# Kernel optimization log

Measured on AMD Instinct MI355X. Metric: run time of the kernel, lower is better.

Reference implementation:

```python
import jax, jax.numpy as jnp
import numpy as np

N_NODES = 100000
N_EDGES = 3200000
EPS = 1e-5


def gcn_conv(x, edge_index, W, b):
    # PyG GCNConv: sym-normalized A+I, transform-then-propagate
    h = x @ W                                   # [N, out]
    src, dst = edge_index[0], edge_index[1]
    ones = jnp.ones(edge_index.shape[1], dtype=x.dtype)
    deg = jax.ops.segment_sum(ones, dst, num_segments=N_NODES) + 1.0  # +1 self-loop
    dis = jax.lax.rsqrt(deg)                    # deg^{-1/2}
    coef = (dis[src] * dis[dst])[:, None]
    agg = jax.ops.segment_sum(h[src] * coef, dst, num_segments=N_NODES)
    agg = agg + h * (dis * dis)[:, None]        # self-loop contribution
    return agg + b


def batch_norm(x, gamma, beta):
    mu = jnp.mean(x, axis=0)
    var = jnp.mean(jnp.square(x - mu), axis=0)
    return (x - mu) * jax.lax.rsqrt(var + EPS) * gamma + beta


def setup_inputs() -> dict:
    key = jax.random.key(0)
    ks = jax.random.split(key, 12)
    d = {
        "x": jax.random.normal(ks[0], (N_NODES, 256), dtype=jnp.float32),
        "edge_index": jax.random.randint(ks[1], (2, N_EDGES), 0, N_NODES, dtype=jnp.int32),
        "W1": jax.random.normal(ks[2], (256, 128), dtype=jnp.float32) * (1.0 / np.sqrt(256)),
        "b1": jnp.zeros((128,), jnp.float32),
        "g1": jnp.ones((128,), jnp.float32),
        "bt1": jnp.zeros((128,), jnp.float32),
        "W2": jax.random.normal(ks[3], (128, 64), dtype=jnp.float32) * (1.0 / np.sqrt(128)),
        "b2": jnp.zeros((64,), jnp.float32),
        "g2": jnp.ones((64,), jnp.float32),
        "bt2": jnp.zeros((64,), jnp.float32),
        "W3": jax.random.normal(ks[4], (64, 32), dtype=jnp.float32) * (1.0 / np.sqrt(64)),
        "b3": jnp.zeros((32,), jnp.float32),
        "g3": jnp.ones((32,), jnp.float32),
        "bt3": jnp.zeros((32,), jnp.float32),
        "Wfc": jax.random.normal(ks[5], (32, 1), dtype=jnp.float32) * (1.0 / np.sqrt(32)),
        "bfc": jnp.zeros((1,), jnp.float32),
    }
    return d


def reference(x, edge_index, W1, b1, g1, bt1, W2, b2, g2, bt2, W3, b3, g3, bt3, Wfc, bfc):
    h = jax.nn.relu(batch_norm(gcn_conv(x, edge_index, W1, b1), g1, bt1))
    h = jax.nn.relu(batch_norm(gcn_conv(h, edge_index, W2, b2), g2, bt2))
    h = jax.nn.relu(batch_norm(gcn_conv(h, edge_index, W3, b3), g3, bt3))
    return h @ Wfc + bfc
```

## Files before the change

### kernel.cpp

```cpp
#include <hip/hip_runtime.h>
#include <hip/hip_fp16.h>

#define EPS 1e-5f
constexpr int NT = 256;
constexpr int BSH = 9;
constexpr int BNODES = 1 << BSH;
constexpr int CH = 4096;
constexpr int PADCAP = 15 * BNODES;

typedef _Float16 v8h __attribute__((ext_vector_type(8)));
typedef float v4f __attribute__((ext_vector_type(4)));


__global__ __launch_bounds__(NT) void bhist_kernel(const int* __restrict__ dst, int* __restrict__ gbhist,
                                                   int E, int NBUK) {
    __shared__ int h[512];
    int tid = threadIdx.x;
    for (int i = tid; i < 512; i += NT) h[i] = 0;
    __syncthreads();
    for (int e = blockIdx.x * NT + tid; e < E; e += gridDim.x * NT)
        atomicAdd(&h[dst[e] >> BSH], 1);
    __syncthreads();
    for (int i = tid; i < NBUK; i += NT)
        if (h[i]) atomicAdd(&gbhist[i], h[i]);
}


__global__ __launch_bounds__(NT) void bscan_kernel(const int* __restrict__ gbhist, int* __restrict__ bbase,
                                                   int* __restrict__ gcur, int E, int NBUK) {
    __shared__ int wsum[5];
    int tid = threadIdx.x;
    int lane = tid & 63, wid = tid >> 6;
    int e0 = (2 * tid < NBUK) ? gbhist[2 * tid] : 0;
    int e1 = (2 * tid + 1 < NBUK) ? gbhist[2 * tid + 1] : 0;
    int u = e0 + e1;
    int incl = u;
    #pragma unroll
    for (int off = 1; off < 64; off <<= 1) {
        int t = __shfl_up(incl, off, 64);
        if (lane >= off) incl += t;
    }
    if (lane == 63) wsum[wid] = incl;
    __syncthreads();
    if (tid == 0) { int s = 0; for (int w = 0; w < 4; w++) { int t = wsum[w]; wsum[w] = s; s += t; } }
    __syncthreads();
    int base = wsum[wid] + incl - u;
    if (2 * tid < NBUK)     { bbase[2 * tid] = base;          gcur[2 * tid] = base; }
    if (2 * tid + 1 < NBUK) { bbase[2 * tid + 1] = base + e0; gcur[2 * tid + 1] = base + e0; }
    if (tid == 0) bbase[NBUK] = E;
}


__device__ __forceinline__ void part_body(int bx, const int* __restrict__ src, const int* __restrict__ dst,
                                          int* __restrict__ gcur, int* __restrict__ ebuf,
                                          int E, int NBUK, char* smem) {
    constexpr int EPT = CH / NT;
    int* hist  = (int*)smem;
    int* lscan = hist + 512;
    int* gbase = lscan + 512;
    int2* stage = (int2*)(gbase + 512);
    int tid = threadIdx.x;
    int lane = tid & 63;
    int e0 = bx * CH;

    for (int i = tid; i < 512; i += NT) hist[i] = 0;
    __syncthreads();

    int2 ed[EPT]; int rank[EPT]; int buk[EPT];
    #pragma unroll
    for (int j = 0; j < EPT; j++) {
        int e = e0 + j * NT + tid;
        if (e < E) {
            ed[j].x = src[e]; ed[j].y = dst[e];
            buk[j] = ed[j].y >> BSH;
            rank[j] = atomicAdd(&hist[buk[j]], 1);
        } else buk[j] = -1;
    }
    __syncthreads();
    if (tid < 64) {
        int bi = tid * 8;
        int v[8]; int s = 0;
        #pragma unroll
        for (int j = 0; j < 8; j++) { v[j] = s; s += hist[bi + j]; }
        int incl = s;
        #pragma unroll
        for (int off = 1; off < 64; off <<= 1) {
            int t = __shfl_up(incl, off, 64);
            if (lane >= off) incl += t;
        }
        int lb = incl - s;
        #pragma unroll
        for (int j = 0; j < 8; j++) lscan[bi + j] = lb + v[j];
    }
    __syncthreads();
    for (int i = tid; i < NBUK; i += NT) {
        int c = hist[i];
        gbase[i] = c ? atomicAdd(&gcur[i], c) : 0;
    }
    #pragma unroll
    for (int j = 0; j < EPT; j++)
        if (buk[j] >= 0) stage[lscan[buk[j]] + rank[j]] = ed[j];
    __syncthreads();
    int cnt = min(E - e0, CH);
    for (int i = tid; i < cnt; i += NT) {
        int2 e = stage[i];
        int b = e.y >> BSH;
        ebuf[gbase[b] + (i - lscan[b])] = ((e.y & (BNODES - 1)) << 18) | e.x;
    }
}


__device__ __forceinline__ void bfill_body(int bx, const int* __restrict__ ebuf, const int* __restrict__ bbase,
                                           int* __restrict__ row_start, int* __restrict__ pdeg,
                                           float* __restrict__ dis, __half* __restrict__ dis_h,
                                           int* __restrict__ csr, int N, char* smem) {
    int* ldeg = (int*)smem;
    int* lrs  = ldeg + 512;
    int* wsum = lrs + 512;
    int tid = threadIdx.x;
    int lane = tid & 63, wid = tid >> 6;
    int b = bx;
    int node0 = b << BSH;
    int nn = min(BNODES, N - node0);
    int beg = bbase[b], end = bbase[b + 1];
    int begp = beg + b * PADCAP;

    for (int i = tid; i < BNODES; i += NT) ldeg[i] = 0;
    __syncthreads();
    for (int i = beg + tid; i < end; i += NT)
        atomicAdd(&ldeg[ebuf[i] >> 18], 1);
    __syncthreads();
    int e0 = ldeg[2 * tid], e1 = ldeg[2 * tid + 1];
    int p0 = (e0 + 15) & ~15, p1 = (e1 + 15) & ~15;
    int u = p0 + p1;
    int incl = u;
    #pragma unroll
    for (int off = 1; off < 64; off <<= 1) {
        int t = __shfl_up(incl, off, 64);
        if (lane >= off) incl += t;
    }
    if (lane == 63) wsum[wid] = incl;
    __syncthreads();
    if (tid == 0) { int s = 0; for (int w = 0; w < 4; w++) { int t = wsum[w]; wsum[w] = s; s += t; } }
    __syncthreads();
    int base = wsum[wid] + incl - u;
    lrs[2 * tid] = base;
    lrs[2 * tid + 1] = base + p0;
    __syncthreads();
    for (int i = tid; i < nn; i += NT) {
        int dg = ldeg[i];
        pdeg[node0 + i] = (dg + 15) & ~15;
        row_start[node0 + i] = begp + lrs[i];
        float dv = rsqrtf((float)dg + 1.0f);
        dis[node0 + i] = dv;
        dis_h[node0 + i] = __float2half(dv);
    }
    if (bx == 0 && tid == 0) dis_h[N] = __float2half(0.f);
    __syncthreads();
    for (int i = tid; i < BNODES; i += NT) ldeg[i] = 0;
    __syncthreads();
    for (int i = beg + tid; i < end; i += NT) {
        int code = ebuf[i];
        int l = code >> 18;
        int off = atomicAdd(&ldeg[l], 1);
        csr[begp + lrs[l] + off] = code & 0x3FFFF;
    }
    __syncthreads();
    for (int i = tid; i < nn; i += NT) {
        int dg = ldeg[i];
        int pd = (dg + 15) & ~15;
        int cbase = begp + lrs[i];
        for (int k = dg; k < pd; k++) csr[cbase + k] = N;
    }
}


__global__ __launch_bounds__(NT) void prepw_kernel(const float* __restrict__ W1, const float* __restrict__ W2,
                                                   const float* __restrict__ W3, __half* __restrict__ Wt1,
                                                   __half* __restrict__ Wt2, __half* __restrict__ Wt3,
                                                   __half* __restrict__ bufA, int N) {
    int i = blockIdx.x * NT + threadIdx.x;
    if (i < 256 * 128) {
        int k = i >> 7, f = i & 127;
        Wt1[f * 256 + k] = __float2half(W1[i]);
    } else if (i < 256 * 128 + 128 * 64) {
        int j = i - 256 * 128; int k = j >> 6, f = j & 63;
        Wt2[f * 128 + k] = __float2half(W2[j]);
    } else if (i < 256 * 128 + 128 * 64 + 64 * 32) {
        int j = i - 256 * 128 - 128 * 64; int k = j >> 5, f = j & 31;
        Wt3[f * 64 + k] = __float2half(W3[j]);
    } else if (i < 256 * 128 + 128 * 64 + 64 * 32 + 128) {
        bufA[(size_t)N * 128 + (i - (256 * 128 + 128 * 64 + 64 * 32))] = __float2half(0.f);
    }
}


template<int K, int F, bool NORM, bool SC>
__device__ __forceinline__ void mgemm_body(int bx, const void* __restrict__ Xv, const __half* __restrict__ Wt,
                                           const float* __restrict__ dis, const float* __restrict__ S1,
                                           const float* __restrict__ S2, const float* __restrict__ g,
                                           const float* __restrict__ bt, __half* __restrict__ out, int N,
                                           char* smem) {
    constexpr int KC = 32;
    constexpr int CG = F / 16;
    constexpr int LDA = KC + 8;
    __half* As = (__half*)smem;
    __half* Bs = (__half*)(smem + 64 * LDA * 2);
    float* as_ = (float*)(smem + 64 * LDA * 2 + F * LDA * 2);
    float* cs_ = as_ + K;

    int tid = threadIdx.x;
    if constexpr (NORM) {
        float inv = 1.0f / (float)N;
        for (int i = tid; i < K; i += NT) {
            float mu = S1[i] * inv;
            float var = fmaxf(S2[i] * inv - mu * mu, 0.f);
            float av = g[i] * rsqrtf(var + EPS);
            as_[i] = av;
            cs_[i] = bt[i] - mu * av;
        }
        __syncthreads();
    }
    int row0 = bx * 64;
    int wid = tid >> 6, lane = tid & 63;
    int quad = lane >> 4, l16 = lane & 15;
    int tr = tid >> 3;
    int tk = (tid & 7) * 4;

    v4f acc[CG];
    #pragma unroll
    for (int gg = 0; gg < CG; gg++) acc[gg] = (v4f)0.f;

    for (int k0 = 0; k0 < K; k0 += KC) {
        #pragma unroll
        for (int r = tr; r < 64; r += 32) {
            int row = row0 + r;
            __half h0, h1, h2, h3;
            if (row < N) {
                if constexpr (NORM) {
                    const __half2* xp = (const __half2*)((const __half*)Xv + (size_t)row * K + k0 + tk);
                    float2 v0 = __half22float2(xp[0]);
                    float2 v1 = __half22float2(xp[1]);
                    h0 = __float2half(fmaxf(v0.x * as_[k0 + tk]     + cs_[k0 + tk],     0.f));
                    h1 = __float2half(fmaxf(v0.y * as_[k0 + tk + 1] + cs_[k0 + tk + 1], 0.f));
                    h2 = __float2half(fmaxf(v1.x * as_[k0 + tk + 2] + cs_[k0 + tk + 2], 0.f));
                    h3 = __float2half(fmaxf(v1.y * as_[k0 + tk + 3] + cs_[k0 + tk + 3], 0.f));
                } else {
                    float4 v = *(const float4*)((const float*)Xv + (size_t)row * K + k0 + tk);
                    h0 = __float2half(v.x); h1 = __float2half(v.y);
                    h2 = __float2half(v.z); h3 = __float2half(v.w);
                }
            } else {
                h0 = h1 = h2 = h3 = __float2half(0.f);
            }
            __half2* dst = (__half2*)&As[r * LDA + tk];
            dst[0] = __halves2half2(h0, h1);
            dst[1] = __halves2half2(h2, h3);
        }
        #pragma unroll
        for (int n = tr; n < F; n += 32) {
            const __half2* wp = (const __half2*)(Wt + (size_t)n * K + k0 + tk);
            __half2* dst = (__half2*)&Bs[n * LDA + tk];
            dst[0] = wp[0];
            dst[1] = wp[1];
        }
        __syncthreads();
        v8h a = *(const v8h*)&As[(wid * 16 + l16) * LDA + quad * 8];
        #pragma unroll
        for (int gg = 0; gg < CG; gg++) {
            v8h b = *(const v8h*)&Bs[(gg * 16 + l16) * LDA + quad * 8];
            acc[gg] = __builtin_amdgcn_mfma_f32_16x16x32_f16(a, b, acc[gg], 0, 0, 0);
        }
        __syncthreads();
    }
    #pragma unroll
    for (int reg = 0; reg < 4; reg++) {
        int row = row0 + wid * 16 + quad * 4 + reg;
        if (row < N) {
            float d = SC ? dis[row] : 1.0f;
            #pragma unroll
            for (int gg = 0; gg < CG; gg++)
                out[(size_t)row * F + gg * 16 + l16] = __float2half(d * acc[gg][reg]);
        } else if (row == N) {
            #pragma unroll
            for (int gg = 0; gg < CG; gg++)
                out[(size_t)row * F + gg * 16 + l16] = __float2half(0.f);
        }
    }
}

template<int K, int F, bool NORM, bool SC>
__global__ __launch_bounds__(NT) void mgemm_kernel(const void* __restrict__ Xv, const __half* __restrict__ Wt,
                                                   const float* __restrict__ dis, const float* __restrict__ S1,
                                                   const float* __restrict__ S2, const float* __restrict__ g,
                                                   const float* __restrict__ bt, __half* __restrict__ out, int N) {
    constexpr int SMB = 64 * 40 * 2 + F * 40 * 2 + (NORM ? 8 * K : 0);
    __shared__ __align__(16) char smem[SMB];
    mgemm_body<K, F, NORM, SC>(blockIdx.x, Xv, Wt, dis, S1, S2, g, bt, out, N, smem);
}


__global__ __launch_bounds__(NT) void fat1_kernel(const int* __restrict__ src, const int* __restrict__ dst,
                                                  int* __restrict__ gcur, int* __restrict__ ebuf, int E, int NBUK,
                                                  int PB, const float* __restrict__ x, const __half* __restrict__ Wt1,
                                                  __half* __restrict__ bufA, int N) {
    __shared__ __align__(16) char smem[38912];
    if ((int)blockIdx.x < PB)
        part_body(blockIdx.x, src, dst, gcur, ebuf, E, NBUK, smem);
    else
        mgemm_body<256, 128, false, false>((int)blockIdx.x - PB, x, Wt1, nullptr, nullptr, nullptr, nullptr,
                                           nullptr, bufA, N, smem);
}

__global__ __launch_bounds__(NT) void fat2_kernel(const int* __restrict__ ebuf, const int* __restrict__ bbase,
                                                  int* __restrict__ row_start, int* __restrict__ pdeg,
                                                  float* __restrict__ dis, __half* __restrict__ dis_h,
                                                  int* __restrict__ csr, const float* __restrict__ x,
                                                  const __half* __restrict__ Wt1, __half* __restrict__ bufA,
                                                  int N, int NBUK, int A) {
    __shared__ __align__(16) char smem[15872];
    if ((int)blockIdx.x < NBUK)
        bfill_body(blockIdx.x, ebuf, bbase, row_start, pdeg, dis, dis_h, csr, N, smem);
    else
        mgemm_body<256, 128, false, false>((int)blockIdx.x - NBUK + A, x, Wt1, nullptr, nullptr, nullptr, nullptr,
                                           nullptr, bufA, N, smem);
}


template<int F, int U, bool DISW>
__global__ __launch_bounds__(NT) void agg_kernel(const __half* __restrict__ hd, const int* __restrict__ csr,
                                                 const int* __restrict__ row_start, const int* __restrict__ pdeg,
                                                 const __half* __restrict__ dis_h, const float* __restrict__ dis,
                                                 const float* __restrict__ b, __half* __restrict__ pre, int N) {
    constexpr int LR = F / 8;
    constexpr int SUBS = 64 / LR;
    constexpr int FSH = (F == 128) ? 7 : (F == 64) ? 6 : 5;
    int node = (blockIdx.x * NT + threadIdx.x) >> 6;
    if (node >= N) return;
    int lane = threadIdx.x & 63;
    int fl = lane % LR, sub = lane / LR;
    int beg = row_start[node];
    int nb = pdeg[node] >> 4;
    int fo = fl * 8;

    __half2 hacc[U][4];
    #pragma unroll
    for (int u = 0; u < U; u++)
        #pragma unroll
        for (int j = 0; j < 4; j++) hacc[u][j] = __half2half2(__half(0.f));

    if (sub == 0) {
        int4 v = *(const int4*)(hd + (((size_t)node << FSH) + fo));
        const __half2* hv = (const __half2*)&v;
        if constexpr (DISW) {
            __half2 dd = __half2half2(dis_h[node]);
            #pragma unroll
            for (int j = 0; j < 4; j++) hacc[0][j] = __hmul2(hv[j], dd);
        } else {
            #pragma unroll
            for (int j = 0; j < 4; j++) hacc[0][j] = hv[j];
        }
    }
    const int* cp = csr + beg + sub;
    int ib = 0;
    for (; ib + 2 <= nb; ib += 2) {
        int s[2 * U];
        #pragma unroll
        for (int u = 0; u < U; u++) {
            s[u]     = cp[u * SUBS];
            s[U + u] = cp[16 + u * SUBS];
        }
        cp += 32;
        int4 v[2 * U];
        __half dv[2 * U];
        #pragma unroll
        for (int t = 0; t < 2 * U; t++) {
            v[t] = *(const int4*)(hd + (((size_t)s[t] << FSH) + fo));
            if constexpr (DISW) dv[t] = dis_h[s[t]];
        }
        #pragma unroll
        for (int t = 0; t < 2 * U; t++) {
            const __half2* hv = (const __half2*)&v[t];
            constexpr int UM = U - 1;
            int u = t & UM;
            if constexpr (DISW) {
                __half2 dd = __half2half2(dv[t]);
                #pragma unroll
                for (int j = 0; j < 4; j++) hacc[u][j] = __hfma2(hv[j], dd, hacc[u][j]);
            } else {
                #pragma unroll
                for (int j = 0; j < 4; j++) hacc[u][j] = __hadd2(hacc[u][j], hv[j]);
            }
        }
    }
    if (ib < nb) {
        int s[U];
        #pragma unroll
        for (int u = 0; u < U; u++) s[u] = cp[u * SUBS];
        int4 v[U];
        __half dv[U];
        #pragma unroll
        for (int u = 0; u < U; u++) {
            v[u] = *(const int4*)(hd + (((size_t)s[u] << FSH) + fo));
            if constexpr (DISW) dv[u] = dis_h[s[u]];
        }
        #pragma unroll
        for (int u = 0; u < U; u++) {
            const __half2* hv = (const __half2*)&v[u];
            if constexpr (DISW) {
                __half2 dd = __half2half2(dv[u]);
                #pragma unroll
                for (int j = 0; j < 4; j++) hacc[u][j] = __hfma2(hv[j], dd, hacc[u][j]);
            } else {
                #pragma unroll
                for (int j = 0; j < 4; j++) hacc[u][j] = __hadd2(hacc[u][j], hv[j]);
            }
        }
    }
    float acc[8];
    #pragma unroll
    for (int j = 0; j < 4; j++) {
        float2 f = __half22float2(hacc[0][j]);
        acc[2 * j] = f.x; acc[2 * j + 1] = f.y;
    }
    #pragma unroll
    for (int u = 1; u < U; u++)
        #pragma unroll
        for (int j = 0; j < 4; j++) {
            float2 f = __half22float2(hacc[u][j]);
            acc[2 * j] += f.x; acc[2 * j + 1] += f.y;
        }
    #pragma unroll
    for (int m = LR; m < 64; m <<= 1)
        #pragma unroll
        for (int j = 0; j < 8; j++) acc[j] += __shfl_xor(acc[j], m, 64);
    if (sub == 0) {
        float d = dis[node];
        float4 b0 = *(const float4*)(b + fo);
        float4 b1 = *(const float4*)(b + fo + 4);
        __half2 h[4];
        h[0] = __floats2half2_rn(d * acc[0] + b0.x, d * acc[1] + b0.y);
        h[1] = __floats2half2_rn(d * acc[2] + b0.z, d * acc[3] + b0.w);
        h[2] = __floats2half2_rn(d * acc[4] + b1.x, d * acc[5] + b1.y);
        h[3] = __floats2half2_rn(d * acc[6] + b1.z, d * acc[7] + b1.w);
        *(int4*)(pre + (((size_t)node << FSH) + fo)) = *(int4*)h;
    }
}


template<int F>
__global__ __launch_bounds__(NT) void stats_kernel(const __half* __restrict__ pre, float* __restrict__ S1,
                                                   float* __restrict__ S2, int N) {
    constexpr int FP = F / 2;
    constexpr int RPB = NT / FP;
    int tid = threadIdx.x;
    int f = tid % FP, r0 = tid / FP;
    float s1x = 0.f, s1y = 0.f, s2x = 0.f, s2y = 0.f;
    const __half2* p2 = (const __half2*)pre;
    for (int node = blockIdx.x * RPB + r0; node < N; node += gridDim.x * RPB) {
        float2 v = __half22float2(p2[(size_t)node * FP + f]);
        s1x += v.x; s1y += v.y; s2x += v.x * v.x; s2y += v.y * v.y;
    }
    __shared__ float l1x[NT], l1y[NT], l2x[NT], l2y[NT];
    l1x[tid] = s1x; l1y[tid] = s1y; l2x[tid] = s2x; l2y[tid] = s2y;
    __syncthreads();
    if (tid < FP) {
        #pragma unroll
        for (int j = 1; j < RPB; j++) {
            s1x += l1x[tid + j * FP]; s1y += l1y[tid + j * FP];
            s2x += l2x[tid + j * FP]; s2y += l2y[tid + j * FP];
        }
        atomicAdd(&S1[2 * tid], s1x); atomicAdd(&S1[2 * tid + 1], s1y);
        atomicAdd(&S2[2 * tid], s2x); atomicAdd(&S2[2 * tid + 1], s2y);
    }
}


__global__ __launch_bounds__(NT) void fc_kernel(const __half* __restrict__ pre, const float* __restrict__ S1,
                                                const float* __restrict__ S2, const float* __restrict__ g,
                                                const float* __restrict__ bt, const float* __restrict__ wfc,
                                                const float* __restrict__ bfc, float* __restrict__ out, int N) {
    __shared__ float wa[32], wc[32], ww[32];
    int tid = threadIdx.x;
    if (tid < 32) {
        float inv = 1.0f / (float)N;
        float mu = S1[tid] * inv;
        float var = fmaxf(S2[tid] * inv - mu * mu, 0.f);
        float av = g[tid] * rsqrtf(var + EPS);
        wa[tid] = av; wc[tid] = bt[tid] - mu * av; ww[tid] = wfc[tid];
    }
    __syncthreads();
    int n = blockIdx.x * NT + tid;
    if (n >= N) return;
    const __half2* p = (const __half2*)(pre + (size_t)n * 32);
    float acc = bfc[0];
    #pragma unroll
    for (int i = 0; i < 16; i++) {
        float2 v = __half22float2(p[i]);
        int f = i * 2;
        acc += fmaxf(v.x * wa[f] + wc[f], 0.f) * ww[f];
        acc += fmaxf(v.y * wa[f + 1] + wc[f + 1], 0.f) * ww[f + 1];
    }
    out[n] = acc;
}


extern "C" void kernel_launch(void* const* d_in, const int* in_sizes, int n_in,
                              void* d_out, int out_size, void* d_ws, size_t ws_size,
                              hipStream_t stream) {
    const float* x   = (const float*)d_in[0];
    const int*   ei  = (const int*)d_in[1];
    const float* W1  = (const float*)d_in[2];
    const float* b1  = (const float*)d_in[3];
    const float* g1  = (const float*)d_in[4];
    const float* bt1 = (const float*)d_in[5];
    const float* W2  = (const float*)d_in[6];
    const float* b2  = (const float*)d_in[7];
    const float* g2  = (const float*)d_in[8];
    const float* bt2 = (const float*)d_in[9];
    const float* W3  = (const float*)d_in[10];
    const float* b3  = (const float*)d_in[11];
    const float* g3  = (const float*)d_in[12];
    const float* bt3 = (const float*)d_in[13];
    const float* Wfc = (const float*)d_in[14];
    const float* bfc = (const float*)d_in[15];
    float* out = (float*)d_out;

    int N = in_sizes[0] / 256;
    int E = in_sizes[1] / 2;
    const int* src = ei;
    const int* dst = ei + E;
    int NBUK = (N + BNODES - 1) >> BSH;

    char* ws = (char*)d_ws;
    size_t off = 0;
    auto alloc = [&](size_t bytes) -> char* {
        char* p = ws + off;
        off += (bytes + 255) & ~(size_t)255;
        return p;
    };
    __half* bufA     = (__half*)alloc((size_t)(N + 1) * 128 * 2);
    __half* bufB     = (__half*)alloc((size_t)N * 128 * 2);
    int*   ebuf      = (int*)alloc((size_t)E * 4);
    int*   csr       = (int*)alloc(((size_t)E + (size_t)NBUK * PADCAP) * 4);
    int*   row_start = (int*)alloc((size_t)N * 4);
    int*   pdeg      = (int*)alloc((size_t)N * 4);
    float* dis       = (float*)alloc((size_t)N * 4);
    __half* dis_h    = (__half*)alloc((size_t)(N + 1) * 2);
    int*   gbhist    = (int*)alloc((size_t)NBUK * 4);
    int*   bbase     = (int*)alloc((size_t)(NBUK + 1) * 4);
    int*   gcur      = (int*)alloc((size_t)NBUK * 4);
    __half* Wt1      = (__half*)alloc(256 * 128 * 2);
    __half* Wt2      = (__half*)alloc(128 * 64 * 2);
    __half* Wt3      = (__half*)alloc(64 * 32 * 2);
    float* stats = (float*)alloc(448 * 4);
    float* S1_1 = stats;       float* S2_1 = S1_1 + 128;
    float* S1_2 = S2_1 + 128;  float* S2_2 = S1_2 + 64;
    float* S1_3 = S2_2 + 64;   float* S2_3 = S1_3 + 32;

    hipMemsetAsync(gbhist, 0, (size_t)NBUK * 4, stream);
    hipMemsetAsync(stats, 0, 448 * 4, stream);

    int GB = (N + 63) / 64;
    int PB = (E + CH - 1) / CH;
    int A = (GB * 3) / 5;
    int AB = (N + 3) / 4;
    int NB = (N + NT - 1) / NT;

    prepw_kernel<<<(256 * 128 + 128 * 64 + 64 * 32 + 128 + NT - 1) / NT, NT, 0, stream>>>(
        W1, W2, W3, Wt1, Wt2, Wt3, bufA, N);
    bhist_kernel<<<512, NT, 0, stream>>>(dst, gbhist, E, NBUK);
    bscan_kernel<<<1, NT, 0, stream>>>(gbhist, bbase, gcur, E, NBUK);
    fat1_kernel<<<PB + A, NT, 0, stream>>>(src, dst, gcur, ebuf, E, NBUK, PB, x, Wt1, bufA, N);
    fat2_kernel<<<NBUK + (GB - A), NT, 0, stream>>>(ebuf, bbase, row_start, pdeg, dis, dis_h, csr,
                                                    x, Wt1, bufA, N, NBUK, A);
    agg_kernel<128, 4, true><<<AB, NT, 0, stream>>>(bufA, csr, row_start, pdeg, dis_h, dis, b1, bufB, N);
    stats_kernel<128><<<256, NT, 0, stream>>>(bufB, S1_1, S2_1, N);
    mgemm_kernel<128, 64, true, true><<<GB, NT, 0, stream>>>(bufB, Wt2, dis, S1_1, S2_1, g1, bt1, bufA, N);
    agg_kernel<64, 2, false><<<AB, NT, 0, stream>>>(bufA, csr, row_start, pdeg, dis_h, dis, b2, bufB, N);
    stats_kernel<64><<<256, NT, 0, stream>>>(bufB, S1_2, S2_2, N);
    mgemm_kernel<64, 32, true, true><<<GB, NT, 0, stream>>>(bufB, Wt3, dis, S1_2, S2_2, g2, bt2, bufA, N);
    agg_kernel<32, 1, false><<<AB, NT, 0, stream>>>(bufA, csr, row_start, pdeg, dis_h, dis, b3, bufB, N);
    stats_kernel<32><<<256, NT, 0, stream>>>(bufB, S1_3, S2_3, N);
    fc_kernel<<<NB, NT, 0, stream>>>(bufB, S1_3, S2_3, g3, bt3, Wfc, bfc, out, N);
}
```

Measured before the change: 600.6 us.

## Fuse post-GEMM1 layer stages into one cooperative persistent kernel with grid syncs

Replaces the nine separate launches for aggregation, batch-norm stats, GEMMs and the final FC with one cooperative persistent kernel. Each stage runs as a grid-stride loop over its work items, and stages are separated by grid.sync with fences. The weight-prep kernel is also merged into the histogram kernel. The aim is to remove launch gaps and tail effects between the short kernels. The cost is that grid-wide barriers and persistent blocks capped by occupancy may lower per-stage parallelism or raise register pressure.

```diff
diff --git a/kernel.cpp b/kernel.cpp
--- a/kernel.cpp
+++ b/kernel.cpp
@@ -1,5 +1,8 @@
 #include <hip/hip_runtime.h>
 #include <hip/hip_fp16.h>
+#include <hip/hip_cooperative_groups.h>
+
+namespace cg = cooperative_groups;
 
 #define EPS 1e-5f
 constexpr int NT = 256;
@@ -12,8 +15,26 @@
 typedef float v4f __attribute__((ext_vector_type(4)));
 
 
-__global__ __launch_bounds__(NT) void bhist_kernel(const int* __restrict__ dst, int* __restrict__ gbhist,
-                                                   int E, int NBUK) {
+__global__ __launch_bounds__(NT) void prep_bhist_kernel(const float* __restrict__ W1, const float* __restrict__ W2,
+                                                        const float* __restrict__ W3, __half* __restrict__ Wt1,
+                                                        __half* __restrict__ Wt2, __half* __restrict__ Wt3,
+                                                        __half* __restrict__ bufA, const int* __restrict__ dst,
+                                                        int* __restrict__ gbhist, int N, int E, int NBUK) {
+    constexpr int TOT = 256 * 128 + 128 * 64 + 64 * 32 + 128;
+    for (int i = blockIdx.x * NT + threadIdx.x; i < TOT; i += gridDim.x * NT) {
+        if (i < 256 * 128) {
+            int k = i >> 7, f = i & 127;
+            Wt1[f * 256 + k] = __float2half(W1[i]);
+        } else if (i < 256 * 128 + 128 * 64) {
+            int j = i - 256 * 128; int k = j >> 6, f = j & 63;
+            Wt2[f * 128 + k] = __float2half(W2[j]);
+        } else if (i < 256 * 128 + 128 * 64 + 64 * 32) {
+            int j = i - 256 * 128 - 128 * 64; int k = j >> 5, f = j & 31;
+            Wt3[f * 64 + k] = __float2half(W3[j]);
+        } else {
+            bufA[(size_t)N * 128 + (i - (256 * 128 + 128 * 64 + 64 * 32))] = __float2half(0.f);
+        }
+    }
     __shared__ int h[512];
     int tid = threadIdx.x;
     for (int i = tid; i < 512; i += NT) h[i] = 0;
@@ -171,26 +192,6 @@
         int pd = (dg + 15) & ~15;
         int cbase = begp + lrs[i];
         for (int k = dg; k < pd; k++) csr[cbase + k] = N;
-    }
-}
-
-
-__global__ __launch_bounds__(NT) void prepw_kernel(const float* __restrict__ W1, const float* __restrict__ W2,
-                                                   const float* __restrict__ W3, __half* __restrict__ Wt1,
-                                                   __half* __restrict__ Wt2, __half* __restrict__ Wt3,
-                                                   __half* __restrict__ bufA, int N) {
-    int i = blockIdx.x * NT + threadIdx.x;
-    if (i < 256 * 128) {
-        int k = i >> 7, f = i & 127;
-        Wt1[f * 256 + k] = __float2half(W1[i]);
-    } else if (i < 256 * 128 + 128 * 64) {
-        int j = i - 256 * 128; int k = j >> 6, f = j & 63;
-        Wt2[f * 128 + k] = __float2half(W2[j]);
-    } else if (i < 256 * 128 + 128 * 64 + 64 * 32) {
-        int j = i - 256 * 128 - 128 * 64; int k = j >> 5, f = j & 31;
-        Wt3[f * 64 + k] = __float2half(W3[j]);
-    } else if (i < 256 * 128 + 128 * 64 + 64 * 32 + 128) {
-        bufA[(size_t)N * 128 + (i - (256 * 128 + 128 * 64 + 64 * 32))] = __float2half(0.f);
     }
 }
 
@@ -289,16 +290,6 @@
     }
 }
 
-template<int K, int F, bool NORM, bool SC>
-__global__ __launch_bounds__(NT) void mgemm_kernel(const void* __restrict__ Xv, const __half* __restrict__ Wt,
-                                                   const float* __restrict__ dis, const float* __restrict__ S1,
-                                                   const float* __restrict__ S2, const float* __restrict__ g,
-                                                   const float* __restrict__ bt, __half* __restrict__ out, int N) {
-    constexpr int SMB = 64 * 40 * 2 + F * 40 * 2 + (NORM ? 8 * K : 0);
-    __shared__ __align__(16) char smem[SMB];
-    mgemm_body<K, F, NORM, SC>(blockIdx.x, Xv, Wt, dis, S1, S2, g, bt, out, N, smem);
-}
-
 
 __global__ __launch_bounds__(NT) void fat1_kernel(const int* __restrict__ src, const int* __restrict__ dst,
                                                   int* __restrict__ gcur, int* __restrict__ ebuf, int E, int NBUK,
@@ -328,14 +319,14 @@
 
 
 template<int F, int U, bool DISW>
-__global__ __launch_bounds__(NT) void agg_kernel(const __half* __restrict__ hd, const int* __restrict__ csr,
-                                                 const int* __restrict__ row_start, const int* __restrict__ pdeg,
-                                                 const __half* __restrict__ dis_h, const float* __restrict__ dis,
-                                                 const float* __restrict__ b, __half* __restrict__ pre, int N) {
+__device__ __forceinline__ void agg_body(int gb, const __half* __restrict__ hd, const int* __restrict__ csr,
+                                         const int* __restrict__ row_start, const int* __restrict__ pdeg,
+                                         const __half* __restrict__ dis_h, const float* __restrict__ dis,
+                                         const float* __restrict__ b, __half* __restrict__ pre, int N) {
     constexpr int LR = F / 8;
     constexpr int SUBS = 64 / LR;
     constexpr int FSH = (F == 128) ? 7 : (F == 64) ? 6 : 5;
-    int node = (blockIdx.x * NT + threadIdx.x) >> 6;
+    int node = gb * 4 + (int)(threadIdx.x >> 6);
     if (node >= N) return;
     int lane = threadIdx.x & 63;
     int fl = lane % LR, sub = lane / LR;
@@ -449,10 +440,14 @@
 
 
 template<int F>
-__global__ __launch_bounds__(NT) void stats_kernel(const __half* __restrict__ pre, float* __restrict__ S1,
-                                                   float* __restrict__ S2, int N) {
+__device__ __forceinline__ void stats_body(const __half* __restrict__ pre, float* __restrict__ S1,
+                                           float* __restrict__ S2, int N, char* smem) {
     constexpr int FP = F / 2;
     constexpr int RPB = NT / FP;
+    float* l1x = (float*)smem;
+    float* l1y = l1x + NT;
+    float* l2x = l1x + 2 * NT;
+    float* l2y = l1x + 3 * NT;
     int tid = threadIdx.x;
     int f = tid % FP, r0 = tid / FP;
     float s1x = 0.f, s1y = 0.f, s2x = 0.f, s2y = 0.f;
@@ -461,7 +456,6 @@
         float2 v = __half22float2(p2[(size_t)node * FP + f]);
         s1x += v.x; s1y += v.y; s2x += v.x * v.x; s2y += v.y * v.y;
     }
-    __shared__ float l1x[NT], l1y[NT], l2x[NT], l2y[NT];
     l1x[tid] = s1x; l1y[tid] = s1y; l2x[tid] = s2x; l2y[tid] = s2y;
     __syncthreads();
     if (tid < FP) {
@@ -473,14 +467,18 @@
         atomicAdd(&S1[2 * tid], s1x); atomicAdd(&S1[2 * tid + 1], s1y);
         atomicAdd(&S2[2 * tid], s2x); atomicAdd(&S2[2 * tid + 1], s2y);
     }
-}
-
-
-__global__ __launch_bounds__(NT) void fc_kernel(const __half* __restrict__ pre, const float* __restrict__ S1,
-                                                const float* __restrict__ S2, const float* __restrict__ g,
-                                                const float* __restrict__ bt, const float* __restrict__ wfc,
-                                                const float* __restrict__ bfc, float* __restrict__ out, int N) {
-    __shared__ float wa[32], wc[32], ww[32];
+    __syncthreads();
+}
+
+
+__device__ __forceinline__ void fc_body(const __half* __restrict__ pre, const float* __restrict__ S1,
+                                        const float* __restrict__ S2, const float* __restrict__ g,
+                                        const float* __restrict__ bt, const float* __restrict__ wfc,
+                                        const float* __restrict__ bfc, float* __restrict__ out, int N,
+                                        char* smem) {
+    float* wa = (float*)smem;
+    float* wc = wa + 32;
+    float* ww = wa + 64;
     int tid = threadIdx.x;
     if (tid < 32) {
         float inv = 1.0f / (float)N;
@@ -490,18 +488,63 @@
         wa[tid] = av; wc[tid] = bt[tid] - mu * av; ww[tid] = wfc[tid];
     }
     __syncthreads();
-    int n = blockIdx.x * NT + tid;
-    if (n >= N) return;
-    const __half2* p = (const __half2*)(pre + (size_t)n * 32);
-    float acc = bfc[0];
-    #pragma unroll
-    for (int i = 0; i < 16; i++) {
-        float2 v = __half22float2(p[i]);
-        int f = i * 2;
-        acc += fmaxf(v.x * wa[f] + wc[f], 0.f) * ww[f];
-        acc += fmaxf(v.y * wa[f + 1] + wc[f + 1], 0.f) * ww[f + 1];
-    }
-    out[n] = acc;
+    for (int n = blockIdx.x * NT + tid; n < N; n += gridDim.x * NT) {
+        const __half2* p = (const __half2*)(pre + (size_t)n * 32);
+        float acc = bfc[0];
+        #pragma unroll
+        for (int i = 0; i < 16; i++) {
+            float2 v = __half22float2(p[i]);
+            int f = i * 2;
+            acc += fmaxf(v.x * wa[f] + wc[f], 0.f) * ww[f];
+            acc += fmaxf(v.y * wa[f + 1] + wc[f + 1], 0.f) * ww[f + 1];
+        }
+        out[n] = acc;
+    }
+}
+
+
+struct MegaP {
+    __half* bufA; __half* bufB;
+    const int* csr; const int* row_start; const int* pdeg;
+    const __half* dis_h; const float* dis;
+    const __half* Wt2; const __half* Wt3;
+    const float* b1; const float* g1; const float* bt1;
+    const float* b2; const float* g2; const float* bt2;
+    const float* b3; const float* g3; const float* bt3;
+    const float* Wfc; const float* bfc;
+    float* S1_1; float* S2_1; float* S1_2; float* S2_2; float* S1_3; float* S2_3;
+    float* out;
+    int N, GB, AB;
+};
+
+__global__ __launch_bounds__(NT, 4) void mega_kernel(MegaP p) {
+    cg::grid_group grid = cg::this_grid();
+    __shared__ __align__(16) char smem[15872];
+    #define GSYNC() do { __threadfence(); grid.sync(); __threadfence(); } while (0)
+
+    for (int gb = blockIdx.x; gb < p.AB; gb += gridDim.x)
+        agg_body<128, 4, true>(gb, p.bufA, p.csr, p.row_start, p.pdeg, p.dis_h, p.dis, p.b1, p.bufB, p.N);
+    GSYNC();
+    stats_body<128>(p.bufB, p.S1_1, p.S2_1, p.N, smem);
+    GSYNC();
+    for (int bx = blockIdx.x; bx < p.GB; bx += gridDim.x)
+        mgemm_body<128, 64, true, true>(bx, p.bufB, p.Wt2, p.dis, p.S1_1, p.S2_1, p.g1, p.bt1, p.bufA, p.N, smem);
+    GSYNC();
+    for (int gb = blockIdx.x; gb < p.AB; gb += gridDim.x)
+        agg_body<64, 2, false>(gb, p.bufA, p.csr, p.row_start, p.pdeg, p.dis_h, p.dis, p.b2, p.bufB, p.N);
+    GSYNC();
+    stats_body<64>(p.bufB, p.S1_2, p.S2_2, p.N, smem);
+    GSYNC();
+    for (int bx = blockIdx.x; bx < p.GB; bx += gridDim.x)
+        mgemm_body<64, 32, true, true>(bx, p.bufB, p.Wt3, p.dis, p.S1_2, p.S2_2, p.g2, p.bt2, p.bufA, p.N, smem);
+    GSYNC();
+    for (int gb = blockIdx.x; gb < p.AB; gb += gridDim.x)
+        agg_body<32, 1, false>(gb, p.bufA, p.csr, p.row_start, p.pdeg, p.dis_h, p.dis, p.b3, p.bufB, p.N);
+    GSYNC();
+    stats_body<32>(p.bufB, p.S1_3, p.S2_3, p.N, smem);
+    GSYNC();
+    fc_body(p.bufB, p.S1_3, p.S2_3, p.g3, p.bt3, p.Wfc, p.bfc, p.out, p.N, smem);
+    #undef GSYNC
 }
 
 
@@ -565,22 +608,38 @@
     int PB = (E + CH - 1) / CH;
     int A = (GB * 3) / 5;
     int AB = (N + 3) / 4;
-    int NB = (N + NT - 1) / NT;
-
-    prepw_kernel<<<(256 * 128 + 128 * 64 + 64 * 32 + 128 + NT - 1) / NT, NT, 0, stream>>>(
-        W1, W2, W3, Wt1, Wt2, Wt3, bufA, N);
-    bhist_kernel<<<512, NT, 0, stream>>>(dst, gbhist, E, NBUK);
+
+    prep_bhist_kernel<<<512, NT, 0, stream>>>(W1, W2, W3, Wt1, Wt2, Wt3, bufA, dst, gbhist, N, E, NBUK);
     bscan_kernel<<<1, NT, 0, stream>>>(gbhist, bbase, gcur, E, NBUK);
     fat1_kernel<<<PB + A, NT, 0, stream>>>(src, dst, gcur, ebuf, E, NBUK, PB, x, Wt1, bufA, N);
     fat2_kernel<<<NBUK + (GB - A), NT, 0, stream>>>(ebuf, bbase, row_start, pdeg, dis, dis_h, csr,
                                                     x, Wt1, bufA, N, NBUK, A);
-    agg_kernel<128, 4, true><<<AB, NT, 0, stream>>>(bufA, csr, row_start, pdeg, dis_h, dis, b1, bufB, N);
-    stats_kernel<128><<<256, NT, 0, stream>>>(bufB, S1_1, S2_1, N);
-    mgemm_kernel<128, 64, true, true><<<GB, NT, 0, stream>>>(bufB, Wt2, dis, S1_1, S2_1, g1, bt1, bufA, N);
-    agg_kernel<64, 2, false><<<AB, NT, 0, stream>>>(bufA, csr, row_start, pdeg, dis_h, dis, b2, bufB, N);
-    stats_kernel<64><<<256, NT, 0, stream>>>(bufB, S1_2, S2_2, N);
-    mgemm_kernel<64, 32, true, true><<<GB, NT, 0, stream>>>(bufB, Wt3, dis, S1_2, S2_2, g2, bt2, bufA, N);
-    agg_kernel<32, 1, false><<<AB, NT, 0, stream>>>(bufA, csr, row_start, pdeg, dis_h, dis, b3, bufB, N);
-    stats_kernel<32><<<256, NT, 0, stream>>>(bufB, S1_3, S2_3, N);
-    fc_kernel<<<NB, NT, 0, stream>>>(bufB, S1_3, S2_3, g3, bt3, Wfc, bfc, out, N);
-}
+
+    static int gblocks = 0;
+    if (gblocks == 0) {
+        int occ = 0;
+        if (hipOccupancyMaxActiveBlocksPerMultiprocessor(&occ, (const void*)mega_kernel, NT, 0) != hipSuccess ||
+            occ < 1)
+            occ = 4;
+        int ncu = 256;
+        hipDeviceProp_t prop;
+        int dev = 0;
+        if (hipGetDevice(&dev) == hipSuccess && hipGetDeviceProperties(&prop, dev) == hipSuccess)
+            ncu = prop.multiProcessorCount;
+        gblocks = ncu * occ;
+    }
+    MegaP p;
+    p.bufA = bufA; p.bufB = bufB;
+    p.csr = csr; p.row_start = row_start; p.pdeg = pdeg;
+    p.dis_h = dis_h; p.dis = dis;
+    p.Wt2 = Wt2; p.Wt3 = Wt3;
+    p.b1 = b1; p.g1 = g1; p.bt1 = bt1;
+    p.b2 = b2; p.g2 = g2; p.bt2 = bt2;
+    p.b3 = b3; p.g3 = g3; p.bt3 = bt3;
+    p.Wfc = Wfc; p.bfc = bfc;
+    p.S1_1 = S1_1; p.S2_1 = S2_1; p.S1_2 = S1_2; p.S2_2 = S2_2; p.S1_3 = S1_3; p.S2_3 = S2_3;
+    p.out = out;
+    p.N = N; p.GB = GB; p.AB = AB;
+    void* kargs[] = { (void*)&p };
+    hipLaunchCooperativeKernel((const void*)mega_kernel, dim3(gblocks), dim3(NT), kargs, 0, stream);
+}
```

Result: slower. 1.769 ms (+194.5%).

## Fuse batch-norm statistics into aggregation epilogue and merge weight prep with histogram

Applied to the files above, without the earlier changes.

The separate stats kernels are removed. Each aggregation block now stages its four output rows in shared memory and adds per-feature sum and sum-of-squares into the global statistics with float atomics. This saves re-reading the pre-activation buffer and three launches. The weight transpose/convert kernel is also folded into the bucket histogram kernel as a grid-stride prologue, saving one more launch. The trade-off is heavy atomic contention: every 4-node block hits the same F addresses, which means tens of thousands of atomics per address. Each aggregation block also gains an extra barrier.

```diff
diff --git a/kernel.cpp b/kernel.cpp
--- a/kernel.cpp
+++ b/kernel.cpp
@@ -12,8 +12,26 @@
 typedef float v4f __attribute__((ext_vector_type(4)));
 
 
-__global__ __launch_bounds__(NT) void bhist_kernel(const int* __restrict__ dst, int* __restrict__ gbhist,
-                                                   int E, int NBUK) {
+__global__ __launch_bounds__(NT) void prep_bhist_kernel(const float* __restrict__ W1, const float* __restrict__ W2,
+                                                        const float* __restrict__ W3, __half* __restrict__ Wt1,
+                                                        __half* __restrict__ Wt2, __half* __restrict__ Wt3,
+                                                        __half* __restrict__ bufA, const int* __restrict__ dst,
+                                                        int* __restrict__ gbhist, int N, int E, int NBUK) {
+    constexpr int TOT = 256 * 128 + 128 * 64 + 64 * 32 + 128;
+    for (int i = blockIdx.x * NT + threadIdx.x; i < TOT; i += gridDim.x * NT) {
+        if (i < 256 * 128) {
+            int k = i >> 7, f = i & 127;
+            Wt1[f * 256 + k] = __float2half(W1[i]);
+        } else if (i < 256 * 128 + 128 * 64) {
+            int j = i - 256 * 128; int k = j >> 6, f = j & 63;
+            Wt2[f * 128 + k] = __float2half(W2[j]);
+        } else if (i < 256 * 128 + 128 * 64 + 64 * 32) {
+            int j = i - 256 * 128 - 128 * 64; int k = j >> 5, f = j & 31;
+            Wt3[f * 64 + k] = __float2half(W3[j]);
+        } else {
+            bufA[(size_t)N * 128 + (i - (256 * 128 + 128 * 64 + 64 * 32))] = __float2half(0.f);
+        }
+    }
     __shared__ int h[512];
     int tid = threadIdx.x;
     for (int i = tid; i < 512; i += NT) h[i] = 0;
@@ -171,26 +189,6 @@
         int pd = (dg + 15) & ~15;
         int cbase = begp + lrs[i];
         for (int k = dg; k < pd; k++) csr[cbase + k] = N;
-    }
-}
-
-
-__global__ __launch_bounds__(NT) void prepw_kernel(const float* __restrict__ W1, const float* __restrict__ W2,
-                                                   const float* __restrict__ W3, __half* __restrict__ Wt1,
-                                                   __half* __restrict__ Wt2, __half* __restrict__ Wt3,
-                                                   __half* __restrict__ bufA, int N) {
-    int i = blockIdx.x * NT + threadIdx.x;
-    if (i < 256 * 128) {
-        int k = i >> 7, f = i & 127;
-        Wt1[f * 256 + k] = __float2half(W1[i]);
-    } else if (i < 256 * 128 + 128 * 64) {
-        int j = i - 256 * 128; int k = j >> 6, f = j & 63;
-        Wt2[f * 128 + k] = __float2half(W2[j]);
-    } else if (i < 256 * 128 + 128 * 64 + 64 * 32) {
-        int j = i - 256 * 128 - 128 * 64; int k = j >> 5, f = j & 31;
-        Wt3[f * 64 + k] = __float2half(W3[j]);
-    } else if (i < 256 * 128 + 128 * 64 + 64 * 32 + 128) {
-        bufA[(size_t)N * 128 + (i - (256 * 128 + 128 * 64 + 64 * 32))] = __float2half(0.f);
     }
 }
 
@@ -331,147 +329,146 @@
 __global__ __launch_bounds__(NT) void agg_kernel(const __half* __restrict__ hd, const int* __restrict__ csr,
                                                  const int* __restrict__ row_start, const int* __restrict__ pdeg,
                                                  const __half* __restrict__ dis_h, const float* __restrict__ dis,
-                                                 const float* __restrict__ b, __half* __restrict__ pre, int N) {
+                                                 const float* __restrict__ b, __half* __restrict__ pre,
+                                                 float* __restrict__ S1, float* __restrict__ S2, int N) {
     constexpr int LR = F / 8;
     constexpr int SUBS = 64 / LR;
     constexpr int FSH = (F == 128) ? 7 : (F == 64) ? 6 : 5;
-    int node = (blockIdx.x * NT + threadIdx.x) >> 6;
-    if (node >= N) return;
-    int lane = threadIdx.x & 63;
+    __shared__ float vbuf[4][F];
+    int tid = threadIdx.x;
+    int wav = tid >> 6;
+    int node = blockIdx.x * 4 + wav;
+    bool active = node < N;
+    int lane = tid & 63;
     int fl = lane % LR, sub = lane / LR;
-    int beg = row_start[node];
-    int nb = pdeg[node] >> 4;
     int fo = fl * 8;
 
-    __half2 hacc[U][4];
-    #pragma unroll
-    for (int u = 0; u < U; u++)
-        #pragma unroll
-        for (int j = 0; j < 4; j++) hacc[u][j] = __half2half2(__half(0.f));
-
-    if (sub == 0) {
-        int4 v = *(const int4*)(hd + (((size_t)node << FSH) + fo));
-        const __half2* hv = (const __half2*)&v;
-        if constexpr (DISW) {
-            __half2 dd = __half2half2(dis_h[node]);
-            #pragma unroll
-            for (int j = 0; j < 4; j++) hacc[0][j] = __hmul2(hv[j], dd);
-        } else {
-            #pragma unroll
-            for (int j = 0; j < 4; j++) hacc[0][j] = hv[j];
-        }
-    }
-    const int* cp = csr + beg + sub;
-    int ib = 0;
-    for (; ib + 2 <= nb; ib += 2) {
-        int s[2 * U];
-        #pragma unroll
-        for (int u = 0; u < U; u++) {
-            s[u]     = cp[u * SUBS];
-            s[U + u] = cp[16 + u * SUBS];
-        }
-        cp += 32;
-        int4 v[2 * U];
-        __half dv[2 * U];
-        #pragma unroll
-        for (int t = 0; t < 2 * U; t++) {
-            v[t] = *(const int4*)(hd + (((size_t)s[t] << FSH) + fo));
-            if constexpr (DISW) dv[t] = dis_h[s[t]];
-        }
-        #pragma unroll
-        for (int t = 0; t < 2 * U; t++) {
-            const __half2* hv = (const __half2*)&v[t];
-            constexpr int UM = U - 1;
-            int u = t & UM;
+    for (int i = tid; i < 4 * F; i += NT) ((float*)vbuf)[i] = 0.f;
+    __syncthreads();
+
+    if (active) {
+        int beg = row_start[node];
+        int nb = pdeg[node] >> 4;
+
+        __half2 hacc[U][4];
+        #pragma unroll
+        for (int u = 0; u < U; u++)
+            #pragma unroll
+            for (int j = 0; j < 4; j++) hacc[u][j] = __half2half2(__half(0.f));
+
+        if (sub == 0) {
+            int4 v = *(const int4*)(hd + (((size_t)node << FSH) + fo));
+            const __half2* hv = (const __half2*)&v;
             if constexpr (DISW) {
-                __half2 dd = __half2half2(dv[t]);
+                __half2 dd = __half2half2(dis_h[node]);
                 #pragma unroll
-                for (int j = 0; j < 4; j++) hacc[u][j] = __hfma2(hv[j], dd, hacc[u][j]);
+                for (int j = 0; j < 4; j++) hacc[0][j] = __hmul2(hv[j], dd);
             } else {
                 #pragma unroll
-                for (int j = 0; j < 4; j++) hacc[u][j] = __hadd2(hacc[u][j], hv[j]);
-            }
-        }
-    }
-    if (ib < nb) {
-        int s[U];
-        #pragma unroll
-        for (int u = 0; u < U; u++) s[u] = cp[u * SUBS];
-        int4 v[U];
-        __half dv[U];
-        #pragma unroll
-        for (int u = 0; u < U; u++) {
-            v[u] = *(const int4*)(hd + (((size_t)s[u] << FSH) + fo));
-            if constexpr (DISW) dv[u] = dis_h[s[u]];
-        }
-        #pragma unroll
-        for (int u = 0; u < U; u++) {
-            const __half2* hv = (const __half2*)&v[u];
-            if constexpr (DISW) {
-                __half2 dd = __half2half2(dv[u]);
-                #pragma unroll
-                for (int j = 0; j < 4; j++) hacc[u][j] = __hfma2(hv[j], dd, hacc[u][j]);
-            } else {
-                #pragma unroll
-                for (int j = 0; j < 4; j++) hacc[u][j] = __hadd2(hacc[u][j], hv[j]);
-            }
-        }
-    }
-    float acc[8];
-    #pragma unroll
-    for (int j = 0; j < 4; j++) {
-        float2 f = __half22float2(hacc[0][j]);
-        acc[2 * j] = f.x; acc[2 * j + 1] = f.y;
-    }
-    #pragma unroll
-    for (int u = 1; u < U; u++)
+                for (int j = 0; j < 4; j++) hacc[0][j] = hv[j];
+            }
+        }
+        const int* cp = csr + beg + sub;
+        int ib = 0;
+        for (; ib + 2 <= nb; ib += 2) {
+            int s[2 * U];
+            #pragma unroll
+            for (int u = 0; u < U; u++) {
+                s[u]     = cp[u * SUBS];
+                s[U + u] = cp[16 + u * SUBS];
+            }
+            cp += 32;
+            int4 v[2 * U];
+            __half dv[2 * U];
+            #pragma unroll
+            for (int t = 0; t < 2 * U; t++) {
+                v[t] = *(const int4*)(hd + (((size_t)s[t] << FSH) + fo));
+                if constexpr (DISW) dv[t] = dis_h[s[t]];
+            }
+            #pragma unroll
+            for (int t = 0; t < 2 * U; t++) {
+                const __half2* hv = (const __half2*)&v[t];
+                constexpr int UM = U - 1;
+                int u = t & UM;
+                if constexpr (DISW) {
+                    __half2 dd = __half2half2(dv[t]);
+                    #pragma unroll
+                    for (int j = 0; j < 4; j++) hacc[u][j] = __hfma2(hv[j], dd, hacc[u][j]);
+                } else {
+                    #pragma unroll
+                    for (int j = 0; j < 4; j++) hacc[u][j] = __hadd2(hacc[u][j], hv[j]);
+                }
+            }
+        }
+        if (ib < nb) {
+            int s[U];
+            #pragma unroll
+            for (int u = 0; u < U; u++) s[u] = cp[u * SUBS];
+            int4 v[U];
+            __half dv[U];
+            #pragma unroll
+            for (int u = 0; u < U; u++) {
+                v[u] = *(const int4*)(hd + (((size_t)s[u] << FSH) + fo));
+                if constexpr (DISW) dv[u] = dis_h[s[u]];
+            }
+            #pragma unroll
+            for (int u = 0; u < U; u++) {
+                const __half2* hv = (const __half2*)&v[u];
+                if constexpr (DISW) {
+                    __half2 dd = __half2half2(dv[u]);
+                    #pragma unroll
+                    for (int j = 0; j < 4; j++) hacc[u][j] = __hfma2(hv[j], dd, hacc[u][j]);
+                } else {
+                    #pragma unroll
+                    for (int j = 0; j < 4; j++) hacc[u][j] = __hadd2(hacc[u][j], hv[j]);
+                }
+            }
+        }
+        float acc[8];
         #pragma unroll
         for (int j = 0; j < 4; j++) {
-            float2 f = __half22float2(hacc[u][j]);
-            acc[2 * j] += f.x; acc[2 * j + 1] += f.y;
-        }
-    #pragma unroll
-    for (int m = LR; m < 64; m <<= 1)
-        #pragma unroll
-        for (int j = 0; j < 8; j++) acc[j] += __shfl_xor(acc[j], m, 64);
-    if (sub == 0) {
-        float d = dis[node];
-        float4 b0 = *(const float4*)(b + fo);
-        float4 b1 = *(const float4*)(b + fo + 4);
-        __half2 h[4];
-        h[0] = __floats2half2_rn(d * acc[0] + b0.x, d * acc[1] + b0.y);
-        h[1] = __floats2half2_rn(d * acc[2] + b0.z, d * acc[3] + b0.w);
-        h[2] = __floats2half2_rn(d * acc[4] + b1.x, d * acc[5] + b1.y);
-        h[3] = __floats2half2_rn(d * acc[6] + b1.z, d * acc[7] + b1.w);
-        *(int4*)(pre + (((size_t)node << FSH) + fo)) = *(int4*)h;
-    }
-}
-
-
-template<int F>
-__global__ __launch_bounds__(NT) void stats_kernel(const __half* __restrict__ pre, float* __restrict__ S1,
-                                                   float* __restrict__ S2, int N) {
-    constexpr int FP = F / 2;
-    constexpr int RPB = NT / FP;
-    int tid = threadIdx.x;
-    int f = tid % FP, r0 = tid / FP;
-    float s1x = 0.f, s1y = 0.f, s2x = 0.f, s2y = 0.f;
-    const __half2* p2 = (const __half2*)pre;
-    for (int node = blockIdx.x * RPB + r0; node < N; node += gridDim.x * RPB) {
-        float2 v = __half22float2(p2[(size_t)node * FP + f]);
-        s1x += v.x; s1y += v.y; s2x += v.x * v.x; s2y += v.y * v.y;
-    }
-    __shared__ float l1x[NT], l1y[NT], l2x[NT], l2y[NT];
-    l1x[tid] = s1x; l1y[tid] = s1y; l2x[tid] = s2x; l2y[tid] = s2y;
-    __syncthreads();
-    if (tid < FP) {
-        #pragma unroll
-        for (int j = 1; j < RPB; j++) {
-            s1x += l1x[tid + j * FP]; s1y += l1y[tid + j * FP];
-            s2x += l2x[tid + j * FP]; s2y += l2y[tid + j * FP];
-        }
-        atomicAdd(&S1[2 * tid], s1x); atomicAdd(&S1[2 * tid + 1], s1y);
-        atomicAdd(&S2[2 * tid], s2x); atomicAdd(&S2[2 * tid + 1], s2y);
+            float2 f = __half22float2(hacc[0][j]);
+            acc[2 * j] = f.x; acc[2 * j + 1] = f.y;
+        }
+        #pragma unroll
+        for (int u = 1; u < U; u++)
+            #pragma unroll
+            for (int j = 0; j < 4; j++) {
+                float2 f = __half22float2(hacc[u][j]);
+                acc[2 * j] += f.x; acc[2 * j + 1] += f.y;
+            }
+        #pragma unroll
+        for (int m = LR; m < 64; m <<= 1)
+            #pragma unroll
+            for (int j = 0; j < 8; j++) acc[j] += __shfl_xor(acc[j], m, 64);
+        if (sub == 0) {
+            float d = dis[node];
+            float4 b0 = *(const float4*)(b + fo);
+            float4 b1 = *(const float4*)(b + fo + 4);
+            __half2 h[4];
+            h[0] = __floats2half2_rn(d * acc[0] + b0.x, d * acc[1] + b0.y);
+            h[1] = __floats2half2_rn(d * acc[2] + b0.z, d * acc[3] + b0.w);
+            h[2] = __floats2half2_rn(d * acc[4] + b1.x, d * acc[5] + b1.y);
+            h[3] = __floats2half2_rn(d * acc[6] + b1.z, d * acc[7] + b1.w);
+            *(int4*)(pre + (((size_t)node << FSH) + fo)) = *(int4*)h;
+            #pragma unroll
+            for (int j = 0; j < 4; j++) {
+                float2 f = __half22float2(h[j]);
+                vbuf[wav][fo + 2 * j]     = f.x;
+                vbuf[wav][fo + 2 * j + 1] = f.y;
+            }
+        }
+    }
+    __syncthreads();
+    if (tid < F) {
+        float s1 = 0.f, s2 = 0.f;
+        #pragma unroll
+        for (int w = 0; w < 4; w++) {
+            float v = vbuf[w][tid];
+            s1 += v; s2 += v * v;
+        }
+        atomicAdd(&S1[tid], s1);
+        atomicAdd(&S2[tid], s2);
     }
 }
 
@@ -567,20 +564,18 @@
     int AB = (N + 3) / 4;
     int NB = (N + NT - 1) / NT;
 
-    prepw_kernel<<<(256 * 128 + 128 * 64 + 64 * 32 + 128 + NT - 1) / NT, NT, 0, stream>>>(
-        W1, W2, W3, Wt1, Wt2, Wt3, bufA, N);
-    bhist_kernel<<<512, NT, 0, stream>>>(dst, gbhist, E, NBUK);
+    prep_bhist_kernel<<<512, NT, 0, stream>>>(W1, W2, W3, Wt1, Wt2, Wt3, bufA, dst, gbhist, N, E, NBUK);
     bscan_kernel<<<1, NT, 0, stream>>>(gbhist, bbase, gcur, E, NBUK);
     fat1_kernel<<<PB + A, NT, 0, stream>>>(src, dst, gcur, ebuf, E, NBUK, PB, x, Wt1, bufA, N);
     fat2_kernel<<<NBUK + (GB - A), NT, 0, stream>>>(ebuf, bbase, row_start, pdeg, dis, dis_h, csr,
                                                     x, Wt1, bufA, N, NBUK, A);
-    agg_kernel<128, 4, true><<<AB, NT, 0, stream>>>(bufA, csr, row_start, pdeg, dis_h, dis, b1, bufB, N);
-    stats_kernel<128><<<256, NT, 0, stream>>>(bufB, S1_1, S2_1, N);
+    agg_kernel<128, 4, true><<<AB, NT, 0, stream>>>(bufA, csr, row_start, pdeg, dis_h, dis, b1, bufB,
+                                                    S1_1, S2_1, N);
     mgemm_kernel<128, 64, true, true><<<GB, NT, 0, stream>>>(bufB, Wt2, dis, S1_1, S2_1, g1, bt1, bufA, N);
-    agg_kernel<64, 2, false><<<AB, NT, 0, stream>>>(bufA, csr, row_start, pdeg, dis_h, dis, b2, bufB, N);
-    stats_kernel<64><<<256, NT, 0, stream>>>(bufB, S1_2, S2_2, N);
+    agg_kernel<64, 2, false><<<AB, NT, 0, stream>>>(bufA, csr, row_start, pdeg, dis_h, dis, b2, bufB,
+                                                    S1_2, S2_2, N);
     mgemm_kernel<64, 32, true, true><<<GB, NT, 0, stream>>>(bufB, Wt3, dis, S1_2, S2_2, g2, bt2, bufA, N);
-    agg_kernel<32, 1, false><<<AB, NT, 0, stream>>>(bufA, csr, row_start, pdeg, dis_h, dis, b3, bufB, N);
-    stats_kernel<32><<<256, NT, 0, stream>>>(bufB, S1_3, S2_3, N);
+    agg_kernel<32, 1, false><<<AB, NT, 0, stream>>>(bufA, csr, row_start, pdeg, dis_h, dis, b3, bufB,
+                                                    S1_3, S2_3, N);
     fc_kernel<<<NB, NT, 0, stream>>>(bufB, S1_3, S2_3, g3, bt3, Wfc, bfc, out, N);
 }
```

Result: slower. 2.141 ms (+256.4%).
